# Kernel tuning notes

Measured on AMD Instinct MI355X. Metric: run time of the kernel, lower is better.

Reference implementation:

```python
import jax, jax.numpy as jnp
import numpy as np

N_NODES = 50000


def _gcn_layer(x, src, dst, W, b, n_nodes):
    # x: [N, Cin] -> linear -> [N, Cout]
    h = x @ W.T + b
    # degree over destination (col) index, including self loops
    deg = jax.ops.segment_sum(jnp.ones(src.shape[0], dtype=x.dtype), dst,
                              num_segments=n_nodes)
    dinv = jnp.where(deg > 0, deg ** -0.5, jnp.zeros((), x.dtype))
    norm = dinv[src] * dinv[dst]                      # [E]
    msg = h[src] * norm[:, None]                      # gather + scale
    return jax.ops.segment_sum(msg, dst, num_segments=n_nodes)  # scatter-add


def setup_inputs() -> dict:
    key = jax.random.key(0)
    k1, k2, k3, k4, k5, k6 = jax.random.split(key, 6)
    num_features = 128
    hidden_dim = 128
    n_edges = 1_600_000
    x = jax.random.normal(k1, (N_NODES, num_features), dtype=jnp.float32)
    edge_index = jax.random.randint(k2, (2, n_edges), 0, N_NODES, dtype=jnp.int64)
    bound1 = 1.0 / np.sqrt(num_features)
    W1 = jax.random.uniform(k3, (hidden_dim, num_features), jnp.float32, -bound1, bound1)
    b1 = jax.random.uniform(k4, (hidden_dim,), jnp.float32, -bound1, bound1)
    bound2 = 1.0 / np.sqrt(hidden_dim)
    W2 = jax.random.uniform(k5, (hidden_dim, hidden_dim), jnp.float32, -bound2, bound2)
    b2 = jax.random.uniform(k6, (hidden_dim,), jnp.float32, -bound2, bound2)
    return {"x": x, "edge_index": edge_index, "W1": W1, "b1": b1, "W2": W2, "b2": b2}


def reference(x, edge_index, W1, b1, W2, b2):
    n_nodes = x.shape[0]
    # add_self_loops: append (i, i) for every node
    loops = jnp.arange(n_nodes, dtype=edge_index.dtype)
    src = jnp.concatenate([edge_index[0], loops])
    dst = jnp.concatenate([edge_index[1], loops])
    h = _gcn_layer(x, src, dst, W1, b1, n_nodes)
    h = jax.nn.relu(h)
    # dropout is identity in eval mode (deterministic reference)
    out = _gcn_layer(h, src, dst, W2, b2, n_nodes)
    return out
```

## Files before the change

### kernel.cpp

```cpp
#include <hip/hip_runtime.h>


static constexpr int F = 128;
static constexpr int NR = 128;
static constexpr int CH = 4096;
static constexpr int CAP = 4608;
static constexpr int RMAX = 512;

typedef __attribute__((ext_vector_type(8))) short bf16x8;
typedef __attribute__((ext_vector_type(4))) float f32x4;
typedef __attribute__((ext_vector_type(4))) unsigned short u16x4;

__device__ __forceinline__ unsigned f2b(float x) {
  unsigned u = __float_as_uint(x);
  return (u + 0x7fffu + ((u >> 16) & 1u)) >> 16;
}
__device__ __forceinline__ float b_lo(unsigned u) {
  return __uint_as_float(u << 16);
}
__device__ __forceinline__ float b_hi(unsigned u) {
  return __uint_as_float(u & 0xffff0000u);
}
__device__ __forceinline__ float b16f(unsigned short v) {
  return __uint_as_float(((unsigned)v) << 16);
}

__global__ void k_initcur(int* __restrict__ gcur, int R) {
  int i = blockIdx.x * blockDim.x + threadIdx.x;
  if (i < R) gcur[i] = i * CAP;
}

__global__ __launch_bounds__(256) void k_part(const int* __restrict__ src,
                                              const int* __restrict__ dst,
                                              int E, int R,
                                              int* __restrict__ gcur,
                                              unsigned* __restrict__ rsorted) {
  __shared__ int h[RMAX];
  __shared__ int cur[RMAX];
  for (int i = threadIdx.x; i < R; i += 256) h[i] = 0;
  __syncthreads();
  const int e0 = blockIdx.x * CH;
  const int e1 = min(e0 + CH, E);
  for (int i = e0 + threadIdx.x; i < e1; i += 256)
    atomicAdd(&h[dst[i] >> 7], 1);
  __syncthreads();
  for (int i = threadIdx.x; i < R; i += 256)
    cur[i] = h[i] ? atomicAdd(&gcur[i], h[i]) : 0;
  __syncthreads();
  for (int i = e0 + threadIdx.x; i < e1; i += 256) {
    const int d = dst[i];
    const int s = src[i];
    const int pos = atomicAdd(&cur[d >> 7], 1);
    rsorted[pos] = ((unsigned)(d & (NR - 1)) << 16) | (unsigned)s;
  }
}

__global__ __launch_bounds__(256) void k_fillR(
    const unsigned* __restrict__ rsorted, const int* __restrict__ gcur,
    int N, int* __restrict__ rowptr, int* __restrict__ rowend,
    float* __restrict__ dinv, unsigned short* __restrict__ csr) {
  __shared__ int cnt[NR];
  __shared__ int sc[NR];
  __shared__ int cur[NR];
  const int r = blockIdx.x;
  const int tid = threadIdx.x;
  const int b = r * CAP;
  const int e = gcur[r];
  if (tid < NR) cnt[tid] = 0;
  __syncthreads();
  for (int i = b + tid; i < e; i += 256)
    atomicAdd(&cnt[rsorted[i] >> 16], 1);
  __syncthreads();
  if (tid < NR) sc[tid] = cnt[tid];
  __syncthreads();
#pragma unroll
  for (int off = 1; off < NR; off <<= 1) {
    int a = (tid < NR && tid >= off) ? sc[tid - off] : 0;
    __syncthreads();
    if (tid < NR) sc[tid] += a;
    __syncthreads();
  }
  if (tid < NR) {
    const int excl = sc[tid] - cnt[tid];
    cur[tid] = excl;
    const int node = r * NR + tid;
    if (node < N) {
      rowptr[node] = b + excl;
      rowend[node] = b + excl + cnt[tid];
      dinv[node] = rsqrtf((float)(cnt[tid] + 1));
    }
  }
  __syncthreads();
  for (int i = b + tid; i < e; i += 256) {
    const unsigned v = rsorted[i];
    const int pos = b + atomicAdd(&cur[v >> 16], 1);
    csr[pos] = (unsigned short)(v & 0xFFFFu);
  }
}

__global__ __launch_bounds__(256) void k_splitW(const float* __restrict__ W,
                                                unsigned short* __restrict__ hi,
                                                unsigned short* __restrict__ lo) {
  const int i = blockIdx.x * 256 + threadIdx.x;
  const int j = i & 7;
  const int lane = (i >> 3) & 63;
  const int f = (i >> 9) & 7;
  const int t = i >> 12;
  const int col = f * 16 + (lane & 15);
  const int k = t * 32 + ((j & 4) << 2) + 4 * (lane >> 4) + (j & 3);
  const float x = W[col * F + k];
  const unsigned h = f2b(x);
  hi[i] = (unsigned short)h;
  lo[i] = (unsigned short)f2b(x - __uint_as_float(h << 16));
}

__global__ __launch_bounds__(256) void k_splitA(const float* __restrict__ A,
                                                unsigned short* __restrict__ hi,
                                                unsigned short* __restrict__ lo,
                                                int n4) {
  const int i = blockIdx.x * 256 + threadIdx.x;
  if (i >= n4) return;
  const float4 v = *(const float4*)(A + (size_t)i * 4);
  u16x4 h, l;
  unsigned u;
  u = f2b(v.x); h[0] = (unsigned short)u; l[0] = (unsigned short)f2b(v.x - __uint_as_float(u << 16));
  u = f2b(v.y); h[1] = (unsigned short)u; l[1] = (unsigned short)f2b(v.y - __uint_as_float(u << 16));
  u = f2b(v.z); h[2] = (unsigned short)u; l[2] = (unsigned short)f2b(v.z - __uint_as_float(u << 16));
  u = f2b(v.w); h[3] = (unsigned short)u; l[3] = (unsigned short)f2b(v.w - __uint_as_float(u << 16));
  *(u16x4*)(hi + (size_t)i * 4) = h;
  *(u16x4*)(lo + (size_t)i * 4) = l;
}

__global__ __launch_bounds__(256) void k_gemm_mfma(
    const unsigned short* __restrict__ Ahi, const unsigned short* __restrict__ Alo,
    const unsigned short* __restrict__ Whi, const unsigned short* __restrict__ Wlo,
    const float* __restrict__ bias, const float* __restrict__ dinv,
    unsigned short* __restrict__ hout, int n) {
  const int wid = threadIdx.x >> 6;
  const int lane = threadIdx.x & 63;
  const int r = lane & 15;
  const int g = lane >> 4;
  const int m0 = blockIdx.x * 64 + wid * 16;
  const int arow = m0 + r;

  f32x4 acc[8];
#pragma unroll
  for (int f = 0; f < 8; ++f) acc[f] = (f32x4){0.f, 0.f, 0.f, 0.f};

#pragma unroll
  for (int t = 0; t < 4; ++t) {
    bf16x8 bhi[8], blo[8];
#pragma unroll
    for (int f = 0; f < 8; ++f) {
      const size_t base = (((size_t)t * 8 + f) * 64 + lane) * 8;
      bhi[f] = *(const bf16x8*)(Whi + base);
      blo[f] = *(const bf16x8*)(Wlo + base);
    }
    const int kt = t * 32;
    bf16x8 ahi = (bf16x8){0, 0, 0, 0, 0, 0, 0, 0};
    bf16x8 alo = (bf16x8){0, 0, 0, 0, 0, 0, 0, 0};
    if (arow < n) {
      const size_t ab = (size_t)arow * F + kt + 4 * g;
      const u16x4 h0 = *(const u16x4*)(Ahi + ab);
      const u16x4 h1 = *(const u16x4*)(Ahi + ab + 16);
      const u16x4 l0 = *(const u16x4*)(Alo + ab);
      const u16x4 l1 = *(const u16x4*)(Alo + ab + 16);
      ahi[0] = (short)h0[0]; ahi[1] = (short)h0[1]; ahi[2] = (short)h0[2]; ahi[3] = (short)h0[3];
      ahi[4] = (short)h1[0]; ahi[5] = (short)h1[1]; ahi[6] = (short)h1[2]; ahi[7] = (short)h1[3];
      alo[0] = (short)l0[0]; alo[1] = (short)l0[1]; alo[2] = (short)l0[2]; alo[3] = (short)l0[3];
      alo[4] = (short)l1[0]; alo[5] = (short)l1[1]; alo[6] = (short)l1[2]; alo[7] = (short)l1[3];
    }
#pragma unroll
    for (int f = 0; f < 8; ++f) {
      acc[f] = __builtin_amdgcn_mfma_f32_16x16x32_bf16(ahi, bhi[f], acc[f], 0, 0, 0);
      acc[f] = __builtin_amdgcn_mfma_f32_16x16x32_bf16(ahi, blo[f], acc[f], 0, 0, 0);
      acc[f] = __builtin_amdgcn_mfma_f32_16x16x32_bf16(alo, bhi[f], acc[f], 0, 0, 0);
    }
  }

  int orow[4];
  float dv[4];
#pragma unroll
  for (int j = 0; j < 4; ++j) {
    orow[j] = m0 + 4 * g + j;
    dv[j] = (orow[j] < n) ? dinv[orow[j]] : 0.f;
  }
#pragma unroll
  for (int f = 0; f < 8; ++f) {
    const int col = f * 16 + r;
    const float bv = bias[col];
#pragma unroll
    for (int j = 0; j < 4; ++j) {
      if (orow[j] < n)
        hout[(size_t)orow[j] * F + col] = (unsigned short)f2b((acc[f][j] + bv) * dv[j]);
    }
  }
}

template <int MODE>
__global__ __launch_bounds__(256) void k_pull(
    const int* __restrict__ rowptr, const int* __restrict__ rowend,
    const unsigned short* __restrict__ csr, const uint2* __restrict__ h,
    const float* __restrict__ dinv, unsigned short* __restrict__ ahi,
    unsigned short* __restrict__ alo, float* __restrict__ fout, int n) {
  const int wid = (blockIdx.x * blockDim.x + threadIdx.x) >> 6;
  if (wid >= n) return;
  const int lane = threadIdx.x & 63;
  const int half = lane >> 5;
  const int l32 = lane & 31;
  const int beg = rowptr[wid];
  const int end = rowend[wid];

  float4 acc = make_float4(0.f, 0.f, 0.f, 0.f);
  if (half == 0) {
    const uint2 u = h[(size_t)wid * 32 + l32];
    acc.x = b_lo(u.x); acc.y = b_hi(u.x);
    acc.z = b_lo(u.y); acc.w = b_hi(u.y);
  }

  int k = beg + half;
  for (; k + 6 < end; k += 8) {
    const int s0 = __builtin_nontemporal_load(csr + k);
    const int s1 = __builtin_nontemporal_load(csr + k + 2);
    const int s2 = __builtin_nontemporal_load(csr + k + 4);
    const int s3 = __builtin_nontemporal_load(csr + k + 6);
    const uint2 u0 = h[(size_t)s0 * 32 + l32];
    const uint2 u1 = h[(size_t)s1 * 32 + l32];
    const uint2 u2 = h[(size_t)s2 * 32 + l32];
    const uint2 u3 = h[(size_t)s3 * 32 + l32];
    acc.x += b_lo(u0.x) + b_lo(u1.x) + b_lo(u2.x) + b_lo(u3.x);
    acc.y += b_hi(u0.x) + b_hi(u1.x) + b_hi(u2.x) + b_hi(u3.x);
    acc.z += b_lo(u0.y) + b_lo(u1.y) + b_lo(u2.y) + b_lo(u3.y);
    acc.w += b_hi(u0.y) + b_hi(u1.y) + b_hi(u2.y) + b_hi(u3.y);
  }
  for (; k < end; k += 2) {
    const uint2 u = h[(size_t)__builtin_nontemporal_load(csr + k) * 32 + l32];
    acc.x += b_lo(u.x);
    acc.y += b_hi(u.x);
    acc.z += b_lo(u.y);
    acc.w += b_hi(u.y);
  }

  acc.x += __shfl_xor(acc.x, 32, 64);
  acc.y += __shfl_xor(acc.y, 32, 64);
  acc.z += __shfl_xor(acc.z, 32, 64);
  acc.w += __shfl_xor(acc.w, 32, 64);

  if (half == 0) {
    const float dv = dinv[wid];
    float rx = acc.x * dv;
    float ry = acc.y * dv;
    float rz = acc.z * dv;
    float rw = acc.w * dv;
    if (MODE == 0) {
      rx = fmaxf(rx, 0.f);
      ry = fmaxf(ry, 0.f);
      rz = fmaxf(rz, 0.f);
      rw = fmaxf(rw, 0.f);
      u16x4 hv, lv;
      unsigned u;
      u = f2b(rx); hv[0] = (unsigned short)u; lv[0] = (unsigned short)f2b(rx - __uint_as_float(u << 16));
      u = f2b(ry); hv[1] = (unsigned short)u; lv[1] = (unsigned short)f2b(ry - __uint_as_float(u << 16));
      u = f2b(rz); hv[2] = (unsigned short)u; lv[2] = (unsigned short)f2b(rz - __uint_as_float(u << 16));
      u = f2b(rw); hv[3] = (unsigned short)u; lv[3] = (unsigned short)f2b(rw - __uint_as_float(u << 16));
      *(u16x4*)(ahi + (size_t)wid * F + l32 * 4) = hv;
      *(u16x4*)(alo + (size_t)wid * F + l32 * 4) = lv;
    } else {
      float* po = fout + (size_t)wid * F + l32 * 4;
      __builtin_nontemporal_store(rx, po);
      __builtin_nontemporal_store(ry, po + 1);
      __builtin_nontemporal_store(rz, po + 2);
      __builtin_nontemporal_store(rw, po + 3);
    }
  }
}

extern "C" void kernel_launch(void* const* d_in, const int* in_sizes, int n_in,
                              void* d_out, int out_size, void* d_ws, size_t ws_size,
                              hipStream_t stream) {
  const float* x  = (const float*)d_in[0];
  const int*   ei = (const int*)d_in[1];
  const float* W1 = (const float*)d_in[2];
  const float* b1 = (const float*)d_in[3];
  const float* W2 = (const float*)d_in[4];
  const float* b2 = (const float*)d_in[5];

  const int N = in_sizes[0] / F;
  const int E = in_sizes[1] / 2;
  const int* src = ei;
  const int* dst = ei + E;
  const int R = (N + NR - 1) / NR;
  const int C = (E + CH - 1) / CH;

  char* ws = (char*)d_ws;
  int*            gcur    = (int*)(ws + (8u << 10));
  float*          dinv    = (float*)(ws + (16u << 10));
  int*            rowptr  = (int*)(ws + (256u << 10));
  int*            rowend  = (int*)(ws + (512u << 10));
  unsigned short* Whi1    = (unsigned short*)(ws + (768u << 10));
  unsigned short* Wlo1    = (unsigned short*)(ws + (800u << 10));
  unsigned short* Whi2    = (unsigned short*)(ws + (832u << 10));
  unsigned short* Wlo2    = (unsigned short*)(ws + (864u << 10));
  unsigned*       rsorted = (unsigned*)(ws + (1u << 20));
  unsigned short* csr     = (unsigned short*)(ws + (9u << 20));
  unsigned short* hbuf    = (unsigned short*)(ws + (16u << 20));
  unsigned short* Ahi     = (unsigned short*)(ws + (32u << 20));
  unsigned short* Alo     = (unsigned short*)(ws + (45u << 20));
  float*          out     = (float*)d_out;

  const int B = 256;
  const int gemmBlocks = (N + 63) / 64;
  const int pullBlocks = (N * 64 + B - 1) / B;
  const int splitBlocks = (N * F / 4 + B - 1) / B;

  k_initcur<<<(R + 255) / 256, B, 0, stream>>>(gcur, R);
  k_part<<<C, B, 0, stream>>>(src, dst, E, R, gcur, rsorted);
  k_fillR<<<R, B, 0, stream>>>(rsorted, gcur, N, rowptr, rowend, dinv, csr);
  k_splitW<<<64, B, 0, stream>>>(W1, Whi1, Wlo1);
  k_splitW<<<64, B, 0, stream>>>(W2, Whi2, Wlo2);
  k_splitA<<<splitBlocks, B, 0, stream>>>(x, Ahi, Alo, N * F / 4);

  k_gemm_mfma<<<gemmBlocks, B, 0, stream>>>(Ahi, Alo, Whi1, Wlo1, b1, dinv,
                                            hbuf, N);
  k_pull<0><<<pullBlocks, B, 0, stream>>>(rowptr, rowend, csr,
                                          (const uint2*)hbuf, dinv, Ahi, Alo,
                                          nullptr, N);

  k_gemm_mfma<<<gemmBlocks, B, 0, stream>>>(Ahi, Alo, Whi2, Wlo2, b2, dinv,
                                            hbuf, N);
  k_pull<1><<<pullBlocks, B, 0, stream>>>(rowptr, rowend, csr,
                                          (const uint2*)hbuf, dinv, nullptr,
                                          nullptr, out, N);
}
```

Measured before the change: 226.0 us.

## Fuse input split into GEMM, LDS two-pass sort in fillR, drop nontemporal hints

The first GEMM now reads fp32 x directly and splits it into bf16 hi/lo in registers, which removes the separate k_splitA launch and its global round-trip. k_fillR stages each bucket segment in LDS and does an extra counting-sort pass by source high byte, so the CSR source indices within each row come out roughly sorted by source. That improves gather locality in the pull kernels. The nontemporal loads and stores in k_pull become plain cached accesses with a vectorized float4 store. In exchange, fillR uses about 37KB of LDS and adds extra passes, and it now clamps the segment length to CAP.

```diff
diff --git a/kernel.cpp b/kernel.cpp
--- a/kernel.cpp
+++ b/kernel.cpp
@@ -20,9 +20,6 @@
 }
 __device__ __forceinline__ float b_hi(unsigned u) {
   return __uint_as_float(u & 0xffff0000u);
-}
-__device__ __forceinline__ float b16f(unsigned short v) {
-  return __uint_as_float(((unsigned)v) << 16);
 }
 
 __global__ void k_initcur(int* __restrict__ gcur, int R) {
@@ -59,23 +56,45 @@
     const unsigned* __restrict__ rsorted, const int* __restrict__ gcur,
     int N, int* __restrict__ rowptr, int* __restrict__ rowend,
     float* __restrict__ dinv, unsigned short* __restrict__ csr) {
+  __shared__ unsigned seg[CAP];
+  __shared__ unsigned seg2[CAP];
+  __shared__ int cnt2[256];
+  __shared__ int cur2[256];
   __shared__ int cnt[NR];
   __shared__ int sc[NR];
   __shared__ int cur[NR];
   const int r = blockIdx.x;
   const int tid = threadIdx.x;
   const int b = r * CAP;
-  const int e = gcur[r];
+  int e = gcur[r];
+  if (e > b + CAP) e = b + CAP;
+  const int len = e - b;
+
+  cnt2[tid] = 0;
   if (tid < NR) cnt[tid] = 0;
   __syncthreads();
-  for (int i = b + tid; i < e; i += 256)
-    atomicAdd(&cnt[rsorted[i] >> 16], 1);
-  __syncthreads();
+  for (int i = tid; i < len; i += 256) {
+    const unsigned v = rsorted[b + i];
+    seg[i] = v;
+    atomicAdd(&cnt2[(v & 0xffffu) >> 8], 1);
+    atomicAdd(&cnt[v >> 16], 1);
+  }
+  __syncthreads();
+  const int v2 = cnt2[tid];
+  __syncthreads();
+#pragma unroll
+  for (int off = 1; off < 256; off <<= 1) {
+    const int a = (tid >= off) ? cnt2[tid - off] : 0;
+    __syncthreads();
+    cnt2[tid] += a;
+    __syncthreads();
+  }
+  cur2[tid] = cnt2[tid] - v2;
   if (tid < NR) sc[tid] = cnt[tid];
   __syncthreads();
 #pragma unroll
   for (int off = 1; off < NR; off <<= 1) {
-    int a = (tid < NR && tid >= off) ? sc[tid - off] : 0;
+    const int a = (tid < NR && tid >= off) ? sc[tid - off] : 0;
     __syncthreads();
     if (tid < NR) sc[tid] += a;
     __syncthreads();
@@ -91,10 +110,16 @@
     }
   }
   __syncthreads();
-  for (int i = b + tid; i < e; i += 256) {
-    const unsigned v = rsorted[i];
-    const int pos = b + atomicAdd(&cur[v >> 16], 1);
-    csr[pos] = (unsigned short)(v & 0xFFFFu);
+  for (int i = tid; i < len; i += 256) {
+    const unsigned v = seg[i];
+    const int p = atomicAdd(&cur2[(v & 0xffffu) >> 8], 1);
+    seg2[p] = v;
+  }
+  __syncthreads();
+  for (int i = tid; i < len; i += 256) {
+    const unsigned v = seg2[i];
+    const int p = atomicAdd(&cur[v >> 16], 1);
+    csr[b + p] = (unsigned short)(v & 0xFFFFu);
   }
 }
 
@@ -114,25 +139,10 @@
   lo[i] = (unsigned short)f2b(x - __uint_as_float(h << 16));
 }
 
-__global__ __launch_bounds__(256) void k_splitA(const float* __restrict__ A,
-                                                unsigned short* __restrict__ hi,
-                                                unsigned short* __restrict__ lo,
-                                                int n4) {
-  const int i = blockIdx.x * 256 + threadIdx.x;
-  if (i >= n4) return;
-  const float4 v = *(const float4*)(A + (size_t)i * 4);
-  u16x4 h, l;
-  unsigned u;
-  u = f2b(v.x); h[0] = (unsigned short)u; l[0] = (unsigned short)f2b(v.x - __uint_as_float(u << 16));
-  u = f2b(v.y); h[1] = (unsigned short)u; l[1] = (unsigned short)f2b(v.y - __uint_as_float(u << 16));
-  u = f2b(v.z); h[2] = (unsigned short)u; l[2] = (unsigned short)f2b(v.z - __uint_as_float(u << 16));
-  u = f2b(v.w); h[3] = (unsigned short)u; l[3] = (unsigned short)f2b(v.w - __uint_as_float(u << 16));
-  *(u16x4*)(hi + (size_t)i * 4) = h;
-  *(u16x4*)(lo + (size_t)i * 4) = l;
-}
-
+template <bool PRESPLIT>
 __global__ __launch_bounds__(256) void k_gemm_mfma(
-    const unsigned short* __restrict__ Ahi, const unsigned short* __restrict__ Alo,
+    const float* __restrict__ Af32, const unsigned short* __restrict__ Ahi,
+    const unsigned short* __restrict__ Alo,
     const unsigned short* __restrict__ Whi, const unsigned short* __restrict__ Wlo,
     const float* __restrict__ bias, const float* __restrict__ dinv,
     unsigned short* __restrict__ hout, int n) {
@@ -160,15 +170,29 @@
     bf16x8 ahi = (bf16x8){0, 0, 0, 0, 0, 0, 0, 0};
     bf16x8 alo = (bf16x8){0, 0, 0, 0, 0, 0, 0, 0};
     if (arow < n) {
-      const size_t ab = (size_t)arow * F + kt + 4 * g;
-      const u16x4 h0 = *(const u16x4*)(Ahi + ab);
-      const u16x4 h1 = *(const u16x4*)(Ahi + ab + 16);
-      const u16x4 l0 = *(const u16x4*)(Alo + ab);
-      const u16x4 l1 = *(const u16x4*)(Alo + ab + 16);
-      ahi[0] = (short)h0[0]; ahi[1] = (short)h0[1]; ahi[2] = (short)h0[2]; ahi[3] = (short)h0[3];
-      ahi[4] = (short)h1[0]; ahi[5] = (short)h1[1]; ahi[6] = (short)h1[2]; ahi[7] = (short)h1[3];
-      alo[0] = (short)l0[0]; alo[1] = (short)l0[1]; alo[2] = (short)l0[2]; alo[3] = (short)l0[3];
-      alo[4] = (short)l1[0]; alo[5] = (short)l1[1]; alo[6] = (short)l1[2]; alo[7] = (short)l1[3];
+      if (PRESPLIT) {
+        const size_t ab = (size_t)arow * F + kt + 4 * g;
+        const u16x4 h0 = *(const u16x4*)(Ahi + ab);
+        const u16x4 h1 = *(const u16x4*)(Ahi + ab + 16);
+        const u16x4 l0 = *(const u16x4*)(Alo + ab);
+        const u16x4 l1 = *(const u16x4*)(Alo + ab + 16);
+        ahi[0] = (short)h0[0]; ahi[1] = (short)h0[1]; ahi[2] = (short)h0[2]; ahi[3] = (short)h0[3];
+        ahi[4] = (short)h1[0]; ahi[5] = (short)h1[1]; ahi[6] = (short)h1[2]; ahi[7] = (short)h1[3];
+        alo[0] = (short)l0[0]; alo[1] = (short)l0[1]; alo[2] = (short)l0[2]; alo[3] = (short)l0[3];
+        alo[4] = (short)l1[0]; alo[5] = (short)l1[1]; alo[6] = (short)l1[2]; alo[7] = (short)l1[3];
+      } else {
+        const float4 a0 = *(const float4*)(Af32 + (size_t)arow * F + kt + 4 * g);
+        const float4 a1 = *(const float4*)(Af32 + (size_t)arow * F + kt + 16 + 4 * g);
+        unsigned h;
+        h = f2b(a0.x); ahi[0] = (short)h; alo[0] = (short)f2b(a0.x - __uint_as_float(h << 16));
+        h = f2b(a0.y); ahi[1] = (short)h; alo[1] = (short)f2b(a0.y - __uint_as_float(h << 16));
+        h = f2b(a0.z); ahi[2] = (short)h; alo[2] = (short)f2b(a0.z - __uint_as_float(h << 16));
+        h = f2b(a0.w); ahi[3] = (short)h; alo[3] = (short)f2b(a0.w - __uint_as_float(h << 16));
+        h = f2b(a1.x); ahi[4] = (short)h; alo[4] = (short)f2b(a1.x - __uint_as_float(h << 16));
+        h = f2b(a1.y); ahi[5] = (short)h; alo[5] = (short)f2b(a1.y - __uint_as_float(h << 16));
+        h = f2b(a1.z); ahi[6] = (short)h; alo[6] = (short)f2b(a1.z - __uint_as_float(h << 16));
+        h = f2b(a1.w); ahi[7] = (short)h; alo[7] = (short)f2b(a1.w - __uint_as_float(h << 16));
+      }
     }
 #pragma unroll
     for (int f = 0; f < 8; ++f) {
@@ -220,10 +244,10 @@
 
   int k = beg + half;
   for (; k + 6 < end; k += 8) {
-    const int s0 = __builtin_nontemporal_load(csr + k);
-    const int s1 = __builtin_nontemporal_load(csr + k + 2);
-    const int s2 = __builtin_nontemporal_load(csr + k + 4);
-    const int s3 = __builtin_nontemporal_load(csr + k + 6);
+    const int s0 = csr[k];
+    const int s1 = csr[k + 2];
+    const int s2 = csr[k + 4];
+    const int s3 = csr[k + 6];
     const uint2 u0 = h[(size_t)s0 * 32 + l32];
     const uint2 u1 = h[(size_t)s1 * 32 + l32];
     const uint2 u2 = h[(size_t)s2 * 32 + l32];
@@ -234,7 +258,7 @@
     acc.w += b_hi(u0.y) + b_hi(u1.y) + b_hi(u2.y) + b_hi(u3.y);
   }
   for (; k < end; k += 2) {
-    const uint2 u = h[(size_t)__builtin_nontemporal_load(csr + k) * 32 + l32];
+    const uint2 u = h[(size_t)csr[k] * 32 + l32];
     acc.x += b_lo(u.x);
     acc.y += b_hi(u.x);
     acc.z += b_lo(u.y);
@@ -266,11 +290,9 @@
       *(u16x4*)(ahi + (size_t)wid * F + l32 * 4) = hv;
       *(u16x4*)(alo + (size_t)wid * F + l32 * 4) = lv;
     } else {
-      float* po = fout + (size_t)wid * F + l32 * 4;
-      __builtin_nontemporal_store(rx, po);
-      __builtin_nontemporal_store(ry, po + 1);
-      __builtin_nontemporal_store(rz, po + 2);
-      __builtin_nontemporal_store(rw, po + 3);
+      float4 rv;
+      rv.x = rx; rv.y = ry; rv.z = rz; rv.w = rw;
+      *(float4*)(fout + (size_t)wid * F + l32 * 4) = rv;
     }
   }
 }
@@ -311,23 +333,21 @@
   const int B = 256;
   const int gemmBlocks = (N + 63) / 64;
   const int pullBlocks = (N * 64 + B - 1) / B;
-  const int splitBlocks = (N * F / 4 + B - 1) / B;
 
   k_initcur<<<(R + 255) / 256, B, 0, stream>>>(gcur, R);
   k_part<<<C, B, 0, stream>>>(src, dst, E, R, gcur, rsorted);
   k_fillR<<<R, B, 0, stream>>>(rsorted, gcur, N, rowptr, rowend, dinv, csr);
   k_splitW<<<64, B, 0, stream>>>(W1, Whi1, Wlo1);
   k_splitW<<<64, B, 0, stream>>>(W2, Whi2, Wlo2);
-  k_splitA<<<splitBlocks, B, 0, stream>>>(x, Ahi, Alo, N * F / 4);
-
-  k_gemm_mfma<<<gemmBlocks, B, 0, stream>>>(Ahi, Alo, Whi1, Wlo1, b1, dinv,
-                                            hbuf, N);
+
+  k_gemm_mfma<false><<<gemmBlocks, B, 0, stream>>>(x, nullptr, nullptr, Whi1,
+                                                   Wlo1, b1, dinv, hbuf, N);
   k_pull<0><<<pullBlocks, B, 0, stream>>>(rowptr, rowend, csr,
                                           (const uint2*)hbuf, dinv, Ahi, Alo,
                                           nullptr, N);
 
-  k_gemm_mfma<<<gemmBlocks, B, 0, stream>>>(Ahi, Alo, Whi2, Wlo2, b2, dinv,
-                                            hbuf, N);
+  k_gemm_mfma<true><<<gemmBlocks, B, 0, stream>>>(nullptr, Ahi, Alo, Whi2,
+                                                  Wlo2, b2, dinv, hbuf, N);
   k_pull<1><<<pullBlocks, B, 0, stream>>>(rowptr, rowend, csr,
                                           (const uint2*)hbuf, dinv, nullptr,
                                           nullptr, out, N);
```

Measured after the change: 205.2 us. -9.2%, faster.
